# Performance work log

Measured on AMD Instinct MI355X. Metric: run time of the kernel, lower is better.

## Reference

```python
import jax, jax.numpy as jnp
import numpy as np


def setup_inputs() -> dict:
    key = jax.random.key(0)
    k1, k2, k3 = jax.random.split(key, 3)
    E = 1_000_000
    EDGE_IN = 64
    IN_CH = 64
    NUM_NODES = 50_000
    edge_features = jax.random.normal(k1, (E, EDGE_IN), dtype=jnp.float32)
    edge_index = jax.random.randint(k2, (2, E), 0, NUM_NODES, dtype=jnp.int64)
    # torch Linear weight: [out_features, in_features]
    bound = 1.0 / np.sqrt(EDGE_IN)
    W = jax.random.uniform(k3, (IN_CH, EDGE_IN), dtype=jnp.float32, minval=-bound, maxval=bound)
    return {"edge_features": edge_features, "edge_index": edge_index,
            "num_nodes": NUM_NODES, "W": W}


def reference(edge_features, edge_index, num_nodes, W):
    row = edge_index[0]
    # edge linear projection (no bias): [E, edge_in] @ [edge_in, in_ch]
    proj = jnp.einsum('ec,oc->eo', edge_features, W)
    # scatter-add edges into source-node buckets
    node_features = jax.ops.segment_sum(proj, row, num_segments=num_nodes)
    return node_features
```

## Files before the change

### kernel.cpp

```cpp
#include <hip/hip_runtime.h>

#define THREADS 256

__global__ __launch_bounds__(THREADS)
void scatter_accum_kernel(const float* __restrict__ X,
                          const int* __restrict__ row_idx,
                          float* __restrict__ acc,
                          int E)
{
    const int lane   = threadIdx.x & 63;
    const int wave_g = blockIdx.x * (THREADS / 64) + (threadIdx.x >> 6);
    const int nwaves = gridDim.x * (THREADS / 64);

    const int chunk = (E + nwaves - 1) / nwaves;
    const int e0 = wave_g * chunk;
    const int e1 = min(e0 + chunk, E);

    int e = e0;
    for (; e + 3 < e1; e += 4) {
        float v0 = X[(size_t)(e + 0) * 64 + lane];
        float v1 = X[(size_t)(e + 1) * 64 + lane];
        float v2 = X[(size_t)(e + 2) * 64 + lane];
        float v3 = X[(size_t)(e + 3) * 64 + lane];
        int r0 = row_idx[e + 0];
        int r1 = row_idx[e + 1];
        int r2 = row_idx[e + 2];
        int r3 = row_idx[e + 3];
        unsafeAtomicAdd(&acc[(size_t)r0 * 64 + lane], v0);
        unsafeAtomicAdd(&acc[(size_t)r1 * 64 + lane], v1);
        unsafeAtomicAdd(&acc[(size_t)r2 * 64 + lane], v2);
        unsafeAtomicAdd(&acc[(size_t)r3 * 64 + lane], v3);
    }
    for (; e < e1; ++e) {
        float v = X[(size_t)e * 64 + lane];
        int r = row_idx[e];
        unsafeAtomicAdd(&acc[(size_t)r * 64 + lane], v);
    }
}

__global__ __launch_bounds__(THREADS)
void project_inplace_kernel(float* __restrict__ nodes,
                            const float* __restrict__ W,
                            int N)
{
    __shared__ float xs[32 * 64];
    const int lane = threadIdx.x & 63;
    const int wave = threadIdx.x >> 6;

    float4 w[16];
    const float4* wsrc = reinterpret_cast<const float4*>(W + lane * 64);
#pragma unroll
    for (int i = 0; i < 16; ++i) w[i] = wsrc[i];

    const int tile = blockIdx.x * 32;
    if (tile >= N) return;

    const float4* gsrc = reinterpret_cast<const float4*>(nodes + (size_t)tile * 64);
    float4* ldst = reinterpret_cast<float4*>(xs);
    const int lim4 = (N - tile) * 16;
#pragma unroll
    for (int i = 0; i < 2; ++i) {
        int idx = threadIdx.x + i * THREADS;
        if (idx < lim4) ldst[idx] = gsrc[idx];
    }
    __syncthreads();

#pragma unroll
    for (int i = 0; i < 8; ++i) {
        const int rl = wave * 8 + i;
        const int r = tile + rl;
        if (r >= N) break;

        const float4* xv = reinterpret_cast<const float4*>(xs + rl * 64);
        float a0 = 0.f, a1 = 0.f, a2 = 0.f, a3 = 0.f;
#pragma unroll
        for (int c4 = 0; c4 < 16; ++c4) {
            float4 x = xv[c4];
            a0 = fmaf(x.x, w[c4].x, a0);
            a1 = fmaf(x.y, w[c4].y, a1);
            a2 = fmaf(x.z, w[c4].z, a2);
            a3 = fmaf(x.w, w[c4].w, a3);
        }
        nodes[(size_t)r * 64 + lane] = (a0 + a1) + (a2 + a3);
    }
}

extern "C" void kernel_launch(void* const* d_in, const int* in_sizes, int n_in,
                              void* d_out, int out_size, void* d_ws, size_t ws_size,
                              hipStream_t stream) {
    const float* edge_features = (const float*)d_in[0];
    const int*   edge_index    = (const int*)d_in[1];
    const float* W             = (const float*)d_in[3];
    float* out = (float*)d_out;

    const int E = in_sizes[1] / 2;
    const int N = out_size / 64;
    const int* row_idx = edge_index;

    hipMemsetAsync(d_out, 0, (size_t)out_size * sizeof(float), stream);

    scatter_accum_kernel<<<2048, THREADS, 0, stream>>>(edge_features, row_idx,
                                                       out, E);
    const int blocks2 = (N + 31) / 32;
    project_inplace_kernel<<<blocks2, THREADS, 0, stream>>>(out, W, N);
}
```

Before: 488.5 us.

## Replace per-edge float atomics with bucketed edge-id binning and per-node gather

```diff
diff --git a/kernel.cpp b/kernel.cpp
--- a/kernel.cpp
+++ b/kernel.cpp
@@ -1,41 +1,60 @@
 #include <hip/hip_runtime.h>
 
 #define THREADS 256
+#define CAP 64
 
 __global__ __launch_bounds__(THREADS)
-void scatter_accum_kernel(const float* __restrict__ X,
-                          const int* __restrict__ row_idx,
-                          float* __restrict__ acc,
-                          int E)
+void bin_kernel(const int* __restrict__ row_idx,
+                int* __restrict__ cnt,
+                int* __restrict__ ids,
+                const float* __restrict__ X,
+                float* __restrict__ out,
+                int E)
 {
-    const int lane   = threadIdx.x & 63;
-    const int wave_g = blockIdx.x * (THREADS / 64) + (threadIdx.x >> 6);
-    const int nwaves = gridDim.x * (THREADS / 64);
+    int e = blockIdx.x * THREADS + threadIdx.x;
+    if (e >= E) return;
+    int r = row_idx[e];
+    int pos = atomicAdd(&cnt[r], 1);
+    if (pos < CAP) {
+        ids[(size_t)r * CAP + pos] = e;
+    } else {
+        for (int c = 0; c < 64; ++c)
+            unsafeAtomicAdd(&out[(size_t)r * 64 + c], X[(size_t)e * 64 + c]);
+    }
+}
 
-    const int chunk = (E + nwaves - 1) / nwaves;
-    const int e0 = wave_g * chunk;
-    const int e1 = min(e0 + chunk, E);
+__global__ __launch_bounds__(THREADS)
+void gather_kernel(const float* __restrict__ X,
+                   const int* __restrict__ ids,
+                   const int* __restrict__ cnt,
+                   float* __restrict__ out,
+                   int N)
+{
+    const int lane = threadIdx.x & 63;
+    const int node = blockIdx.x * (THREADS / 64) + (threadIdx.x >> 6);
+    if (node >= N) return;
 
-    int e = e0;
-    for (; e + 3 < e1; e += 4) {
-        float v0 = X[(size_t)(e + 0) * 64 + lane];
-        float v1 = X[(size_t)(e + 1) * 64 + lane];
-        float v2 = X[(size_t)(e + 2) * 64 + lane];
-        float v3 = X[(size_t)(e + 3) * 64 + lane];
-        int r0 = row_idx[e + 0];
-        int r1 = row_idx[e + 1];
-        int r2 = row_idx[e + 2];
-        int r3 = row_idx[e + 3];
-        unsafeAtomicAdd(&acc[(size_t)r0 * 64 + lane], v0);
-        unsafeAtomicAdd(&acc[(size_t)r1 * 64 + lane], v1);
-        unsafeAtomicAdd(&acc[(size_t)r2 * 64 + lane], v2);
-        unsafeAtomicAdd(&acc[(size_t)r3 * 64 + lane], v3);
+    const int n = min(cnt[node], CAP);
+    const int* myids = ids + (size_t)node * CAP;
+
+    float acc = out[(size_t)node * 64 + lane];
+
+    int i = 0;
+    for (; i + 3 < n; i += 4) {
+        int e0 = myids[i + 0];
+        int e1 = myids[i + 1];
+        int e2 = myids[i + 2];
+        int e3 = myids[i + 3];
+        float v0 = X[(size_t)e0 * 64 + lane];
+        float v1 = X[(size_t)e1 * 64 + lane];
+        float v2 = X[(size_t)e2 * 64 + lane];
+        float v3 = X[(size_t)e3 * 64 + lane];
+        acc += (v0 + v1) + (v2 + v3);
     }
-    for (; e < e1; ++e) {
-        float v = X[(size_t)e * 64 + lane];
-        int r = row_idx[e];
-        unsafeAtomicAdd(&acc[(size_t)r * 64 + lane], v);
-    }
+    for (; i < n; ++i)
+        acc += X[(size_t)myids[i] * 64 + lane];
+
+    out[(size_t)node * 64 + lane] = acc;
 }
 
 __global__ __launch_bounds__(THREADS)
@@ -85,6 +104,25 @@
     }
 }
 
+__global__ __launch_bounds__(THREADS)
+void scatter_accum_kernel(const float* __restrict__ X,
+                          const int* __restrict__ row_idx,
+                          float* __restrict__ acc,
+                          int E)
+{
+    const int lane   = threadIdx.x & 63;
+    const int wave_g = blockIdx.x * (THREADS / 64) + (threadIdx.x >> 6);
+    const int nwaves = gridDim.x * (THREADS / 64);
+    const int chunk = (E + nwaves - 1) / nwaves;
+    const int e0 = wave_g * chunk;
+    const int e1 = min(e0 + chunk, E);
+    for (int e = e0; e < e1; ++e) {
+        float v = X[(size_t)e * 64 + lane];
+        int r = row_idx[e];
+        unsafeAtomicAdd(&acc[(size_t)r * 64 + lane], v);
+    }
+}
+
 extern "C" void kernel_launch(void* const* d_in, const int* in_sizes, int n_in,
                               void* d_out, int out_size, void* d_ws, size_t ws_size,
                               hipStream_t stream) {
@@ -97,10 +135,25 @@
     const int N = out_size / 64;
     const int* row_idx = edge_index;
 
+    const size_t cnt_bytes = ((size_t)N * sizeof(int) + 255) & ~(size_t)255;
+    const size_t ids_bytes = (size_t)N * CAP * sizeof(int);
+    const bool use_csr = (ws_size >= cnt_bytes + ids_bytes);
+
     hipMemsetAsync(d_out, 0, (size_t)out_size * sizeof(float), stream);
 
-    scatter_accum_kernel<<<2048, THREADS, 0, stream>>>(edge_features, row_idx,
-                                                       out, E);
-    const int blocks2 = (N + 31) / 32;
-    project_inplace_kernel<<<blocks2, THREADS, 0, stream>>>(out, W, N);
+    if (use_csr) {
+        int* cnt = (int*)d_ws;
+        int* ids = (int*)((char*)d_ws + cnt_bytes);
+        hipMemsetAsync(cnt, 0, (size_t)N * sizeof(int), stream);
+
+        bin_kernel<<<(E + THREADS - 1) / THREADS, THREADS, 0, stream>>>(
+            row_idx, cnt, ids, edge_features, out, E);
+        gather_kernel<<<(N + 3) / 4, THREADS, 0, stream>>>(
+            edge_features, ids, cnt, out, N);
+    } else {
+        scatter_accum_kernel<<<2048, THREADS, 0, stream>>>(edge_features,
+                                                           row_idx, out, E);
+    }
+
+    project_inplace_kernel<<<(N + 31) / 32, THREADS, 0, stream>>>(out, W, N);
 }
```

Result: faster. 467.5 us (-4.3%).
